# Kernel tuning notes

Measured on AMD Instinct MI355X. Metric: run time of the kernel, lower is better.

The kernel has to match this reference:

```python
import jax, jax.numpy as jnp
import numpy as np

B, N, IN_F = 8, 1024, 512
H, D = 4, 128  # num_heads, out_features; H*D == IN_F for residual
LN_EPS = 1e-5
NEG_INF = -1e9


def setup_inputs() -> dict:
    key = jax.random.key(0)
    ks = jax.random.split(key, 7)
    x = jax.random.normal(ks[0], (B, N, IN_F), dtype=jnp.float32)
    mask = jax.random.randint(ks[1], (B, N), 0, 2, dtype=jnp.int32)
    # xavier-uniform-ish init scales
    W = jax.random.uniform(ks[2], (IN_F, H * D), dtype=jnp.float32, minval=-1.0, maxval=1.0) * (1.414 * np.sqrt(6.0 / (IN_F + H * D)))
    a_src = jax.random.uniform(ks[3], (H, D), dtype=jnp.float32, minval=-1.0, maxval=1.0) * (1.414 * np.sqrt(6.0 / (H + D)))
    a_dst = jax.random.uniform(ks[4], (H, D), dtype=jnp.float32, minval=-1.0, maxval=1.0) * (1.414 * np.sqrt(6.0 / (H + D)))
    gamma = jnp.ones((H * D,), dtype=jnp.float32)
    beta = jnp.zeros((H * D,), dtype=jnp.float32)
    return {"x": x, "mask": mask, "W": W, "a_src": a_src, "a_dst": a_dst, "gamma": gamma, "beta": beta}


def _layernorm(y, gamma, beta):
    mu = jnp.mean(y, axis=-1, keepdims=True)
    var = jnp.var(y, axis=-1, keepdims=True)
    return (y - mu) * jax.lax.rsqrt(var + LN_EPS) * gamma + beta


def reference(x, mask, W, a_src, a_dst, gamma, beta):
    b, n, _ = x.shape
    h = (x @ W).reshape(b, n, H, D)                      # [B,N,H,D]
    e_i = jnp.einsum('bnhd,hd->bnh', h, a_src)           # [B,N,H]
    e_j = jnp.einsum('bnhd,hd->bnh', h, a_dst)           # [B,N,H]
    e = jax.nn.leaky_relu(e_i[:, :, None, :] + e_j[:, None, :, :], 0.2)  # [B,N,N,H]
    mm = mask[:, None, :, None] * mask[:, :, None, None]  # [B,N,N,1]
    e = jnp.where(mm == 0, NEG_INF, e)
    attn = jax.nn.softmax(e, axis=2)                     # softmax over neighbors j
    h_prime = jnp.einsum('bnjh,bjhd->bnhd', attn, h).reshape(b, n, H * D)
    return _layernorm(h_prime + x, gamma, beta)
```

## Files before the change

kernel.cpp:

```cpp
#include <hip/hip_runtime.h>
#include <math.h>

#define Bsz 8
#define Nn 1024
#define Ff 512
#define Hh 4
#define Dd 128

typedef float f32x4 __attribute__((ext_vector_type(4)));
typedef short bf16x8 __attribute__((ext_vector_type(8)));

__device__ inline uint f2b1(float a) {
    union { float f; uint u; } v; v.f = a;
    return (v.u + 0x7fffu + ((v.u >> 16) & 1u)) >> 16;
}
__device__ inline uint f2b_pk(float a, float b) { return f2b1(a) | (f2b1(b) << 16); }


__global__ __launch_bounds__(256) void conv_xw(const float* __restrict__ X,
                                               const float* __restrict__ Wm,
                                               ushort* __restrict__ Xc,
                                               ushort* __restrict__ Wc) {
    __shared__ float tile[8 * 520];
    const int bi = blockIdx.x, tid = threadIdx.x;
    if (bi < 512) {
        const int mtile = (bi & 7) * 64 + (bi >> 3);
        const int kblk = tid >> 2, m15b = (tid & 3) * 4;
        #pragma unroll
        for (int c = 0; c < 4; ++c) {
            int m15 = m15b + c;
            const float4* xp = (const float4*)(X + (size_t)(mtile * 16 + m15) * Ff + kblk * 8);
            float4 f0 = xp[0], f1 = xp[1];
            uint4 o = { f2b_pk(f0.x, f0.y), f2b_pk(f0.z, f0.w),
                        f2b_pk(f1.x, f1.y), f2b_pk(f1.z, f1.w) };
            *(uint4*)(Xc + (((size_t)(mtile * 64 + kblk) * 16 + m15) << 3)) = o;
        }
    } else {
        const int kb = bi - 512;
        const int l = tid & 63, wv = tid >> 6;
        const int col0 = l * 8;
        #pragma unroll
        for (int rsel = 0; rsel < 2; ++rsel) {
            int kr = wv + rsel * 4;
            const float4* wp = (const float4*)(Wm + (size_t)(kb * 8 + kr) * Ff + col0);
            float4 a = wp[0], c = wp[1];
            *(float4*)(&tile[kr * 520 + col0]) = a;
            *(float4*)(&tile[kr * 520 + col0 + 4]) = c;
        }
        __syncthreads();
        #pragma unroll
        for (int rsel = 0; rsel < 2; ++rsel) {
            int n = tid + rsel * 256;
            float v[8];
            #pragma unroll
            for (int u = 0; u < 8; ++u) v[u] = tile[u * 520 + n];
            uint4 o = { f2b_pk(v[0], v[1]), f2b_pk(v[2], v[3]),
                        f2b_pk(v[4], v[5]), f2b_pk(v[6], v[7]) };
            int nc = n >> 7, nt = (n >> 4) & 7, n15 = n & 15;
            *(uint4*)(Wc + ((size_t)(((nc * 64 + kb) * 8 + nt) * 16 + n15) << 3)) = o;
        }
    }
}

__global__ __launch_bounds__(256, 2) void gemm_xw(const ushort* __restrict__ Xc,
                                                  const ushort* __restrict__ Wc,
                                                  const float* __restrict__ a_src,
                                                  const float* __restrict__ a_dst,
                                                  ushort* __restrict__ hT,
                                                  float* __restrict__ ei,
                                                  float* __restrict__ ej) {
    const int idx = blockIdx.x;
    const int b = idx & 7, sub = idx >> 3;
    const int mi = sub & 15, nc = sub >> 4;
    const int tid = threadIdx.x;
    const int w = tid >> 6, lane = tid & 63, quad = lane >> 4, l16 = lane & 15;
    const int mtile = (b * 16 + mi) * 4 + w;

    f32x4 z = {0.f, 0.f, 0.f, 0.f};
    f32x4 acc[8];
    #pragma unroll
    for (int nt = 0; nt < 8; ++nt) acc[nt] = z;

    const ushort* ap = Xc + ((size_t)mtile << 13) + quad * 128 + l16 * 8;
    const ushort* bp = Wc + ((size_t)nc << 16) + quad * 1024 + l16 * 8;

    bf16x8 ab[2];
    bf16x8 bb[2][8];
    ab[0] = *(const bf16x8*)(ap);
    ab[1] = *(const bf16x8*)(ap + 512);
    #pragma unroll
    for (int nt = 0; nt < 8; ++nt) {
        bb[0][nt] = *(const bf16x8*)(bp + nt * 128);
        bb[1][nt] = *(const bf16x8*)(bp + 4096 + nt * 128);
    }

    #pragma unroll 2
    for (int s = 0; s < 16; ++s) {
        const int c = s & 1;
        #pragma unroll
        for (int nt = 0; nt < 8; ++nt)
            acc[nt] = __builtin_amdgcn_mfma_f32_16x16x32_bf16(ab[c], bb[c][nt], acc[nt], 0, 0, 0);
        if (s + 2 < 16) {
            ab[c] = *(const bf16x8*)(ap + (s + 2) * 512);
            #pragma unroll
            for (int nt = 0; nt < 8; ++nt)
                bb[c][nt] = *(const bf16x8*)(bp + (s + 2) * 4096 + nt * 128);
        }
    }

    const int nseq = (mi * 4 + w) * 16 + quad * 4;
    const int jb = nseq >> 5, js = nseq & 31;
    #pragma unroll
    for (int nt = 0; nt < 8; ++nt) {
        uint2 pv;
        pv.x = f2b_pk(acc[nt][0], acc[nt][1]);
        pv.y = f2b_pk(acc[nt][2], acc[nt][3]);
        int hd = nc * 128 + nt * 16 + l16;
        *(uint2*)(hT + ((size_t)(b * 32 + jb)) * 16384 + (size_t)hd * 32 + js) = pv;
    }

    {
        float as4[8], ad4[8];
        #pragma unroll
        for (int nt = 0; nt < 8; ++nt) {
            as4[nt] = a_src[nc * 128 + nt * 16 + l16];
            ad4[nt] = a_dst[nc * 128 + nt * 16 + l16];
        }
        #pragma unroll
        for (int rr = 0; rr < 4; ++rr) {
            float v1 = 0.f, v2 = 0.f;
            #pragma unroll
            for (int nt = 0; nt < 8; ++nt) {
                v1 += acc[nt][rr] * as4[nt];
                v2 += acc[nt][rr] * ad4[nt];
            }
            #pragma unroll
            for (int off = 1; off < 16; off <<= 1) {
                v1 += __shfl_xor(v1, off);
                v2 += __shfl_xor(v2, off);
            }
            if (l16 == 0) {
                int n = nseq + rr;
                ei[((b * 4 + nc) << 10) + n] = v1;
                ej[((b * 4 + nc) << 10) + n] = v2;
            }
        }
    }
}

__global__ __launch_bounds__(512, 2) void attn_pv(const ushort* __restrict__ hT,
                                                  const float* __restrict__ ei_g,
                                                  const float* __restrict__ ej_g,
                                                  const int* __restrict__ mask,
                                                  const float* __restrict__ X,
                                                  const float* __restrict__ gamma,
                                                  const float* __restrict__ beta,
                                                  float* __restrict__ out) {
    __shared__ float s_ep[32 * 516];
    __shared__ float s_as[4][32];

    const int idx = blockIdx.x;
    const int b = idx & 7, i0 = (idx >> 3) * 32;
    const int tid = threadIdx.x;
    const int w = tid >> 6, w4 = w & 3, jh = w >> 2;
    const int lane = tid & 63, quad = lane >> 4, l16 = lane & 15;

    const float* ejh = ej_g + ((b * 4 + w4) << 10);
    const int* mkb = mask + (b << 10);

    float maxej = -3.0e38f;
    #pragma unroll
    for (int k = 0; k < 16; ++k) maxej = fmaxf(maxej, ejh[lane + 64 * k]);
    #pragma unroll
    for (int off = 1; off < 64; off <<= 1) maxej = fmaxf(maxej, __shfl_xor(maxej, off));

    const float ei0 = ei_g[((b * 4 + w4) << 10) + i0 + l16];
    const float ei1 = ei_g[((b * 4 + w4) << 10) + i0 + 16 + l16];
    const int mi0 = mkb[i0 + l16];
    const int mi1 = mkb[i0 + 16 + l16];
    float m0, m1;
    { float t = ei0 + maxej; m0 = mi0 ? fmaxf(t, 0.2f * t) : -1e9f; }
    { float t = ei1 + maxej; m1 = mi1 ? fmaxf(t, 0.2f * t) : -1e9f; }

    f32x4 z = {0.f, 0.f, 0.f, 0.f};
    f32x4 acc[2][8], asum[2];
    #pragma unroll
    for (int it = 0; it < 2; ++it) { asum[it] = z;
        #pragma unroll
        for (int dt = 0; dt < 8; ++dt) acc[it][dt] = z; }
    bf16x8 ones;
    #pragma unroll
    for (int q = 0; q < 8; ++q) ones[q] = (short)0x3F80;

    const ushort* hTb = hT + ((size_t)(b * 32)) * 16384 + (size_t)(w4 * 128) * 32
                        + l16 * 32 + quad * 8;

    bf16x8 B[2][8];
    #pragma unroll
    for (int c = 0; c < 2; ++c) {
        const ushort* h0 = hTb + (size_t)(jh * 16 + c) * 16384;
        #pragma unroll
        for (int dt = 0; dt < 8; ++dt) B[c][dt] = *(const bf16x8*)(h0 + dt * 512);
    }

    #pragma unroll 2
    for (int r = 0; r < 16; ++r) {
        const int c = r & 1;
        const int jq = (jh * 16 + r) * 32 + quad * 8;
        float4 e0 = *(const float4*)(ejh + jq);
        float4 e1 = *(const float4*)(ejh + jq + 4);
        int4 q0 = *(const int4*)(mkb + jq);
        int4 q1 = *(const int4*)(mkb + jq + 4);
        float ev[8] = {e0.x, e0.y, e0.z, e0.w, e1.x, e1.y, e1.z, e1.w};
        int   mv[8] = {q0.x, q0.y, q0.z, q0.w, q1.x, q1.y, q1.z, q1.w};
        float wv0[8], wv1[8];
        #pragma unroll
        for (int u = 0; u < 8; ++u) {
            float t0 = ei0 + ev[u];
            float l0 = fmaxf(t0, 0.2f * t0);
            wv0[u] = __expf(((mi0 && mv[u]) ? l0 : -1e9f) - m0);
            float t1 = ei1 + ev[u];
            float l1 = fmaxf(t1, 0.2f * t1);
            wv1[u] = __expf(((mi1 && mv[u]) ? l1 : -1e9f) - m1);
        }
        union { uint4 u; bf16x8 v; } af0, af1;
        af0.u.x = f2b_pk(wv0[0], wv0[1]); af0.u.y = f2b_pk(wv0[2], wv0[3]);
        af0.u.z = f2b_pk(wv0[4], wv0[5]); af0.u.w = f2b_pk(wv0[6], wv0[7]);
        af1.u.x = f2b_pk(wv1[0], wv1[1]); af1.u.y = f2b_pk(wv1[2], wv1[3]);
        af1.u.z = f2b_pk(wv1[4], wv1[5]); af1.u.w = f2b_pk(wv1[6], wv1[7]);
        asum[0] = __builtin_amdgcn_mfma_f32_16x16x32_bf16(af0.v, ones, asum[0], 0, 0, 0);
        asum[1] = __builtin_amdgcn_mfma_f32_16x16x32_bf16(af1.v, ones, asum[1], 0, 0, 0);
        #pragma unroll
        for (int dt = 0; dt < 8; ++dt) {
            acc[0][dt] = __builtin_amdgcn_mfma_f32_16x16x32_bf16(af0.v, B[c][dt], acc[0][dt], 0, 0, 0);
            acc[1][dt] = __builtin_amdgcn_mfma_f32_16x16x32_bf16(af1.v, B[c][dt], acc[1][dt], 0, 0, 0);
        }
        if (r + 2 < 16) {
            const ushort* hn = hTb + (size_t)(jh * 16 + r + 2) * 16384;
            #pragma unroll
            for (int dt = 0; dt < 8; ++dt) B[c][dt] = *(const bf16x8*)(hn + dt * 512);
        }
    }

    if (jh == 1) {
        #pragma unroll
        for (int it = 0; it < 2; ++it)
            #pragma unroll
            for (int dt = 0; dt < 8; ++dt)
                #pragma unroll
                for (int rr = 0; rr < 4; ++rr)
                    s_ep[(it * 16 + quad * 4 + rr) * 516 + w4 * 128 + dt * 16 + l16] =
                        acc[it][dt][rr];
        if (l16 == 0) {
            #pragma unroll
            for (int it = 0; it < 2; ++it)
                #pragma unroll
                for (int rr = 0; rr < 4; ++rr)
                    s_as[w4][it * 16 + quad * 4 + rr] = asum[it][rr];
        }
    }
    __syncthreads();
    if (jh == 0) {
        float rs[2][4];
        #pragma unroll
        for (int it = 0; it < 2; ++it)
            #pragma unroll
            for (int rr = 0; rr < 4; ++rr)
                rs[it][rr] = 1.f / (asum[it][rr] + s_as[w4][it * 16 + quad * 4 + rr]);
        #pragma unroll
        for (int it = 0; it < 2; ++it)
            #pragma unroll
            for (int dt = 0; dt < 8; ++dt)
                #pragma unroll
                for (int rr = 0; rr < 4; ++rr) {
                    int off = (it * 16 + quad * 4 + rr) * 516 + w4 * 128 + dt * 16 + l16;
                    s_ep[off] = (acc[it][dt][rr] + s_ep[off]) * rs[it][rr];
                }
    }
    __syncthreads();

    #pragma unroll
    for (int q = 0; q < 4; ++q) {
        int ir = w * 4 + q;
        int ig = i0 + ir;
        float4 p0 = *(const float4*)(&s_ep[ir * 516 + lane * 8]);
        float4 p1 = *(const float4*)(&s_ep[ir * 516 + lane * 8 + 4]);
        const float* xp = X + (((size_t)((b << 10) + ig)) << 9) + lane * 8;
        float4 x0 = *(const float4*)(xp);
        float4 x1 = *(const float4*)(xp + 4);
        float v[8] = {p0.x + x0.x, p0.y + x0.y, p0.z + x0.z, p0.w + x0.w,
                      p1.x + x1.x, p1.y + x1.y, p1.z + x1.z, p1.w + x1.w};
        float s1 = 0.f, s2 = 0.f;
        #pragma unroll
        for (int u = 0; u < 8; ++u) { s1 += v[u]; s2 += v[u] * v[u]; }
        #pragma unroll
        for (int off = 1; off < 64; off <<= 1) { s1 += __shfl_xor(s1, off); s2 += __shfl_xor(s2, off); }
        float mean = s1 * (1.f / 512.f);
        float var  = s2 * (1.f / 512.f) - mean * mean;
        float rstd = rsqrtf(var + 1e-5f);
        int f0i = lane * 8;
        float4 g0 = *(const float4*)(gamma + f0i);
        float4 g1 = *(const float4*)(gamma + f0i + 4);
        float4 be0 = *(const float4*)(beta + f0i);
        float4 be1 = *(const float4*)(beta + f0i + 4);
        float* op = out + (((size_t)((b << 10) + ig)) << 9) + f0i;
        float4 o0, o1;
        o0.x = (v[0] - mean) * rstd * g0.x + be0.x;
        o0.y = (v[1] - mean) * rstd * g0.y + be0.y;
        o0.z = (v[2] - mean) * rstd * g0.z + be0.z;
        o0.w = (v[3] - mean) * rstd * g0.w + be0.w;
        o1.x = (v[4] - mean) * rstd * g1.x + be1.x;
        o1.y = (v[5] - mean) * rstd * g1.y + be1.y;
        o1.z = (v[6] - mean) * rstd * g1.z + be1.z;
        o1.w = (v[7] - mean) * rstd * g1.w + be1.w;
        *(float4*)op = o0;
        *(float4*)(op + 4) = o1;
    }
}

extern "C" void kernel_launch(void* const* d_in, const int* in_sizes, int n_in,
                              void* d_out, int out_size, void* d_ws, size_t ws_size,
                              hipStream_t stream) {
    const float* x     = (const float*)d_in[0];
    const int*   mask  = (const int*)d_in[1];
    const float* W     = (const float*)d_in[2];
    const float* a_src = (const float*)d_in[3];
    const float* a_dst = (const float*)d_in[4];
    const float* gamma = (const float*)d_in[5];
    const float* beta  = (const float*)d_in[6];
    float* out = (float*)d_out;

    ushort* hT = (ushort*)d_ws;
    ushort* Xc = hT + (size_t)8 * 512 * 1024;
    ushort* Wc = Xc + (size_t)8 * 1024 * 512;
    float* ei = (float*)(Wc + (size_t)512 * 512);
    float* ej = ei + 32768;

    conv_xw<<<dim3(576), 256, 0, stream>>>(x, W, Xc, Wc);
    gemm_xw<<<dim3(512), 256, 0, stream>>>(Xc, Wc, a_src, a_dst, hT, ei, ej);
    attn_pv<<<dim3(256), 512, 0, stream>>>(hT, ei, ej, mask, x, gamma, beta, out);
}
```

Before: 125.9 us.

## Fuse three kernels into one cooperative kernel with grid syncs

Result: slower. 204.9 us (+62.8%).

```diff
diff --git a/kernel.cpp b/kernel.cpp
--- a/kernel.cpp
+++ b/kernel.cpp
@@ -1,5 +1,8 @@
 #include <hip/hip_runtime.h>
+#include <hip/hip_cooperative_groups.h>
 #include <math.h>
+
+namespace cg = cooperative_groups;
 
 #define Bsz 8
 #define Nn 1024
@@ -17,15 +20,33 @@
 __device__ inline uint f2b_pk(float a, float b) { return f2b1(a) | (f2b1(b) << 16); }
 
 
-__global__ __launch_bounds__(256) void conv_xw(const float* __restrict__ X,
-                                               const float* __restrict__ Wm,
-                                               ushort* __restrict__ Xc,
-                                               ushort* __restrict__ Wc) {
+__global__ __launch_bounds__(512, 2) void fused_gat(const float* __restrict__ X,
+                                                    const int*   __restrict__ mask,
+                                                    const float* __restrict__ Wm,
+                                                    const float* __restrict__ a_src,
+                                                    const float* __restrict__ a_dst,
+                                                    const float* __restrict__ gamma,
+                                                    const float* __restrict__ beta,
+                                                    float* __restrict__ out,
+                                                    ushort* __restrict__ hT,
+                                                    ushort* __restrict__ Xc,
+                                                    ushort* __restrict__ Wc,
+                                                    float* __restrict__ ei_g,
+                                                    float* __restrict__ ej_g) {
     __shared__ float tile[8 * 520];
-    const int bi = blockIdx.x, tid = threadIdx.x;
-    if (bi < 512) {
-        const int mtile = (bi & 7) * 64 + (bi >> 3);
-        const int kblk = tid >> 2, m15b = (tid & 3) * 4;
+    __shared__ float s_ep[32 * 516];
+    __shared__ float s_as[4][32];
+
+    cg::grid_group grid = cg::this_grid();
+    const int idx = blockIdx.x;
+    const int tid = threadIdx.x;
+    const int b = idx & 7;
+
+    {
+        const int s = idx >> 3;
+        const int half = tid >> 8, t = tid & 255;
+        const int mtile = b * 64 + s * 2 + half;
+        const int kblk = t >> 2, m15b = (t & 3) * 4;
         #pragma unroll
         for (int c = 0; c < 4; ++c) {
             int m15 = m15b + c;
@@ -35,22 +56,15 @@
                         f2b_pk(f1.x, f1.y), f2b_pk(f1.z, f1.w) };
             *(uint4*)(Xc + (((size_t)(mtile * 64 + kblk) * 16 + m15) << 3)) = o;
         }
-    } else {
-        const int kb = bi - 512;
-        const int l = tid & 63, wv = tid >> 6;
-        const int col0 = l * 8;
-        #pragma unroll
-        for (int rsel = 0; rsel < 2; ++rsel) {
-            int kr = wv + rsel * 4;
+        if (idx < 64) {
+            const int kb = idx;
+            const int kr = tid >> 6, col0 = (tid & 63) * 8;
             const float4* wp = (const float4*)(Wm + (size_t)(kb * 8 + kr) * Ff + col0);
             float4 a = wp[0], c = wp[1];
             *(float4*)(&tile[kr * 520 + col0]) = a;
             *(float4*)(&tile[kr * 520 + col0 + 4]) = c;
-        }
-        __syncthreads();
-        #pragma unroll
-        for (int rsel = 0; rsel < 2; ++rsel) {
-            int n = tid + rsel * 256;
+            __syncthreads();
+            const int n = tid;
             float v[8];
             #pragma unroll
             for (int u = 0; u < 8; ++u) v[u] = tile[u * 520 + n];
@@ -60,261 +74,244 @@
             *(uint4*)(Wc + ((size_t)(((nc * 64 + kb) * 8 + nt) * 16 + n15) << 3)) = o;
         }
     }
-}
-
-__global__ __launch_bounds__(256, 2) void gemm_xw(const ushort* __restrict__ Xc,
-                                                  const ushort* __restrict__ Wc,
-                                                  const float* __restrict__ a_src,
-                                                  const float* __restrict__ a_dst,
-                                                  ushort* __restrict__ hT,
-                                                  float* __restrict__ ei,
-                                                  float* __restrict__ ej) {
-    const int idx = blockIdx.x;
-    const int b = idx & 7, sub = idx >> 3;
-    const int mi = sub & 15, nc = sub >> 4;
-    const int tid = threadIdx.x;
-    const int w = tid >> 6, lane = tid & 63, quad = lane >> 4, l16 = lane & 15;
-    const int mtile = (b * 16 + mi) * 4 + w;
-
-    f32x4 z = {0.f, 0.f, 0.f, 0.f};
-    f32x4 acc[8];
-    #pragma unroll
-    for (int nt = 0; nt < 8; ++nt) acc[nt] = z;
-
-    const ushort* ap = Xc + ((size_t)mtile << 13) + quad * 128 + l16 * 8;
-    const ushort* bp = Wc + ((size_t)nc << 16) + quad * 1024 + l16 * 8;
-
-    bf16x8 ab[2];
-    bf16x8 bb[2][8];
-    ab[0] = *(const bf16x8*)(ap);
-    ab[1] = *(const bf16x8*)(ap + 512);
-    #pragma unroll
-    for (int nt = 0; nt < 8; ++nt) {
-        bb[0][nt] = *(const bf16x8*)(bp + nt * 128);
-        bb[1][nt] = *(const bf16x8*)(bp + 4096 + nt * 128);
+    grid.sync();
+
+    {
+        const int w8 = tid >> 6;
+        const int lane = tid & 63, quad = lane >> 4, l16 = lane & 15;
+        const int mi = (idx >> 3) & 15, ncp = idx >> 7;
+        const int nc = ncp * 2 + (w8 >> 2), w = w8 & 3;
+        const int mtile = (b * 16 + mi) * 4 + w;
+
+        f32x4 z = {0.f, 0.f, 0.f, 0.f};
+        f32x4 acc[8];
+        #pragma unroll
+        for (int nt = 0; nt < 8; ++nt) acc[nt] = z;
+
+        const ushort* ap = Xc + ((size_t)mtile << 13) + quad * 128 + l16 * 8;
+        const ushort* bp = Wc + ((size_t)nc << 16) + quad * 1024 + l16 * 8;
+
+        bf16x8 ab[2];
+        bf16x8 bb[2][8];
+        ab[0] = *(const bf16x8*)(ap);
+        ab[1] = *(const bf16x8*)(ap + 512);
+        #pragma unroll
+        for (int nt = 0; nt < 8; ++nt) {
+            bb[0][nt] = *(const bf16x8*)(bp + nt * 128);
+            bb[1][nt] = *(const bf16x8*)(bp + 4096 + nt * 128);
+        }
+
+        #pragma unroll 2
+        for (int s = 0; s < 16; ++s) {
+            const int c = s & 1;
+            #pragma unroll
+            for (int nt = 0; nt < 8; ++nt)
+                acc[nt] = __builtin_amdgcn_mfma_f32_16x16x32_bf16(ab[c], bb[c][nt], acc[nt], 0, 0, 0);
+            if (s + 2 < 16) {
+                ab[c] = *(const bf16x8*)(ap + (s + 2) * 512);
+                #pragma unroll
+                for (int nt = 0; nt < 8; ++nt)
+                    bb[c][nt] = *(const bf16x8*)(bp + (s + 2) * 4096 + nt * 128);
+            }
+        }
+
+        const int nseq = (mi * 4 + w) * 16 + quad * 4;
+        const int jb = nseq >> 5, js = nseq & 31;
+        #pragma unroll
+        for (int nt = 0; nt < 8; ++nt) {
+            uint2 pv;
+            pv.x = f2b_pk(acc[nt][0], acc[nt][1]);
+            pv.y = f2b_pk(acc[nt][2], acc[nt][3]);
+            int hd = nc * 128 + nt * 16 + l16;
+            *(uint2*)(hT + ((size_t)(b * 32 + jb)) * 16384 + (size_t)hd * 32 + js) = pv;
+        }
+
+        {
+            float as4[8], ad4[8];
+            #pragma unroll
+            for (int nt = 0; nt < 8; ++nt) {
+                as4[nt] = a_src[nc * 128 + nt * 16 + l16];
+                ad4[nt] = a_dst[nc * 128 + nt * 16 + l16];
+            }
+            #pragma unroll
+            for (int rr = 0; rr < 4; ++rr) {
+                float v1 = 0.f, v2 = 0.f;
+                #pragma unroll
+                for (int nt = 0; nt < 8; ++nt) {
+                    v1 += acc[nt][rr] * as4[nt];
+                    v2 += acc[nt][rr] * ad4[nt];
+                }
+                #pragma unroll
+                for (int off = 1; off < 16; off <<= 1) {
+                    v1 += __shfl_xor(v1, off);
+                    v2 += __shfl_xor(v2, off);
+                }
+                if (l16 == 0) {
+                    int n = nseq + rr;
+                    ei_g[((b * 4 + nc) << 10) + n] = v1;
+                    ej_g[((b * 4 + nc) << 10) + n] = v2;
+                }
+            }
+        }
     }
-
-    #pragma unroll 2
-    for (int s = 0; s < 16; ++s) {
-        const int c = s & 1;
-        #pragma unroll
-        for (int nt = 0; nt < 8; ++nt)
-            acc[nt] = __builtin_amdgcn_mfma_f32_16x16x32_bf16(ab[c], bb[c][nt], acc[nt], 0, 0, 0);
-        if (s + 2 < 16) {
-            ab[c] = *(const bf16x8*)(ap + (s + 2) * 512);
-            #pragma unroll
-            for (int nt = 0; nt < 8; ++nt)
-                bb[c][nt] = *(const bf16x8*)(bp + (s + 2) * 4096 + nt * 128);
-        }
-    }
-
-    const int nseq = (mi * 4 + w) * 16 + quad * 4;
-    const int jb = nseq >> 5, js = nseq & 31;
-    #pragma unroll
-    for (int nt = 0; nt < 8; ++nt) {
-        uint2 pv;
-        pv.x = f2b_pk(acc[nt][0], acc[nt][1]);
-        pv.y = f2b_pk(acc[nt][2], acc[nt][3]);
-        int hd = nc * 128 + nt * 16 + l16;
-        *(uint2*)(hT + ((size_t)(b * 32 + jb)) * 16384 + (size_t)hd * 32 + js) = pv;
-    }
+    grid.sync();
 
     {
-        float as4[8], ad4[8];
-        #pragma unroll
-        for (int nt = 0; nt < 8; ++nt) {
-            as4[nt] = a_src[nc * 128 + nt * 16 + l16];
-            ad4[nt] = a_dst[nc * 128 + nt * 16 + l16];
-        }
-        #pragma unroll
-        for (int rr = 0; rr < 4; ++rr) {
-            float v1 = 0.f, v2 = 0.f;
-            #pragma unroll
-            for (int nt = 0; nt < 8; ++nt) {
-                v1 += acc[nt][rr] * as4[nt];
-                v2 += acc[nt][rr] * ad4[nt];
-            }
-            #pragma unroll
-            for (int off = 1; off < 16; off <<= 1) {
-                v1 += __shfl_xor(v1, off);
-                v2 += __shfl_xor(v2, off);
-            }
+        const int i0 = (idx >> 3) * 32;
+        const int w = tid >> 6, w4 = w & 3, jh = w >> 2;
+        const int lane = tid & 63, quad = lane >> 4, l16 = lane & 15;
+
+        const float* ejh = ej_g + ((b * 4 + w4) << 10);
+        const int* mkb = mask + (b << 10);
+
+        float maxej = -3.0e38f;
+        #pragma unroll
+        for (int k = 0; k < 16; ++k) maxej = fmaxf(maxej, ejh[lane + 64 * k]);
+        #pragma unroll
+        for (int off = 1; off < 64; off <<= 1) maxej = fmaxf(maxej, __shfl_xor(maxej, off));
+
+        const float ei0 = ei_g[((b * 4 + w4) << 10) + i0 + l16];
+        const float ei1 = ei_g[((b * 4 + w4) << 10) + i0 + 16 + l16];
+        const int mi0 = mkb[i0 + l16];
+        const int mi1 = mkb[i0 + 16 + l16];
+        float m0, m1;
+        { float t = ei0 + maxej; m0 = mi0 ? fmaxf(t, 0.2f * t) : -1e9f; }
+        { float t = ei1 + maxej; m1 = mi1 ? fmaxf(t, 0.2f * t) : -1e9f; }
+
+        f32x4 z = {0.f, 0.f, 0.f, 0.f};
+        f32x4 acc[2][8], asum[2];
+        #pragma unroll
+        for (int it = 0; it < 2; ++it) { asum[it] = z;
+            #pragma unroll
+            for (int dt = 0; dt < 8; ++dt) acc[it][dt] = z; }
+        bf16x8 ones;
+        #pragma unroll
+        for (int q = 0; q < 8; ++q) ones[q] = (short)0x3F80;
+
+        const ushort* hTb = hT + ((size_t)(b * 32)) * 16384 + (size_t)(w4 * 128) * 32
+                            + l16 * 32 + quad * 8;
+
+        bf16x8 B[2][8];
+        #pragma unroll
+        for (int c = 0; c < 2; ++c) {
+            const ushort* h0 = hTb + (size_t)(jh * 16 + c) * 16384;
+            #pragma unroll
+            for (int dt = 0; dt < 8; ++dt) B[c][dt] = *(const bf16x8*)(h0 + dt * 512);
+        }
+
+        #pragma unroll 2
+        for (int r = 0; r < 16; ++r) {
+            const int c = r & 1;
+            const int jq = (jh * 16 + r) * 32 + quad * 8;
+            float4 e0 = *(const float4*)(ejh + jq);
+            float4 e1 = *(const float4*)(ejh + jq + 4);
+            int4 q0 = *(const int4*)(mkb + jq);
+            int4 q1 = *(const int4*)(mkb + jq + 4);
+            float ev[8] = {e0.x, e0.y, e0.z, e0.w, e1.x, e1.y, e1.z, e1.w};
+            int   mv[8] = {q0.x, q0.y, q0.z, q0.w, q1.x, q1.y, q1.z, q1.w};
+            float wv0[8], wv1[8];
+            #pragma unroll
+            for (int u = 0; u < 8; ++u) {
+                float t0 = ei0 + ev[u];
+                float l0 = fmaxf(t0, 0.2f * t0);
+                wv0[u] = __expf(((mi0 && mv[u]) ? l0 : -1e9f) - m0);
+                float t1 = ei1 + ev[u];
+                float l1 = fmaxf(t1, 0.2f * t1);
+                wv1[u] = __expf(((mi1 && mv[u]) ? l1 : -1e9f) - m1);
+            }
+            union { uint4 u; bf16x8 v; } af0, af1;
+            af0.u.x = f2b_pk(wv0[0], wv0[1]); af0.u.y = f2b_pk(wv0[2], wv0[3]);
+            af0.u.z = f2b_pk(wv0[4], wv0[5]); af0.u.w = f2b_pk(wv0[6], wv0[7]);
+            af1.u.x = f2b_pk(wv1[0], wv1[1]); af1.u.y = f2b_pk(wv1[2], wv1[3]);
+            af1.u.z = f2b_pk(wv1[4], wv1[5]); af1.u.w = f2b_pk(wv1[6], wv1[7]);
+            asum[0] = __builtin_amdgcn_mfma_f32_16x16x32_bf16(af0.v, ones, asum[0], 0, 0, 0);
+            asum[1] = __builtin_amdgcn_mfma_f32_16x16x32_bf16(af1.v, ones, asum[1], 0, 0, 0);
+            #pragma unroll
+            for (int dt = 0; dt < 8; ++dt) {
+                acc[0][dt] = __builtin_amdgcn_mfma_f32_16x16x32_bf16(af0.v, B[c][dt], acc[0][dt], 0, 0, 0);
+                acc[1][dt] = __builtin_amdgcn_mfma_f32_16x16x32_bf16(af1.v, B[c][dt], acc[1][dt], 0, 0, 0);
+            }
+            if (r + 2 < 16) {
+                const ushort* hn = hTb + (size_t)(jh * 16 + r + 2) * 16384;
+                #pragma unroll
+                for (int dt = 0; dt < 8; ++dt) B[c][dt] = *(const bf16x8*)(hn + dt * 512);
+            }
+        }
+
+        if (jh == 1) {
+            #pragma unroll
+            for (int it = 0; it < 2; ++it)
+                #pragma unroll
+                for (int dt = 0; dt < 8; ++dt)
+                    #pragma unroll
+                    for (int rr = 0; rr < 4; ++rr)
+                        s_ep[(it * 16 + quad * 4 + rr) * 516 + w4 * 128 + dt * 16 + l16] =
+                            acc[it][dt][rr];
             if (l16 == 0) {
-                int n = nseq + rr;
-                ei[((b * 4 + nc) << 10) + n] = v1;
-                ej[((b * 4 + nc) << 10) + n] = v2;
-            }
-        }
-    }
-}
-
-__global__ __launch_bounds__(512, 2) void attn_pv(const ushort* __restrict__ hT,
-                                                  const float* __restrict__ ei_g,
-                                                  const float* __restrict__ ej_g,
-                                                  const int* __restrict__ mask,
-                                                  const float* __restrict__ X,
-                                                  const float* __restrict__ gamma,
-                                                  const float* __restrict__ beta,
-                                                  float* __restrict__ out) {
-    __shared__ float s_ep[32 * 516];
-    __shared__ float s_as[4][32];
-
-    const int idx = blockIdx.x;
-    const int b = idx & 7, i0 = (idx >> 3) * 32;
-    const int tid = threadIdx.x;
-    const int w = tid >> 6, w4 = w & 3, jh = w >> 2;
-    const int lane = tid & 63, quad = lane >> 4, l16 = lane & 15;
-
-    const float* ejh = ej_g + ((b * 4 + w4) << 10);
-    const int* mkb = mask + (b << 10);
-
-    float maxej = -3.0e38f;
-    #pragma unroll
-    for (int k = 0; k < 16; ++k) maxej = fmaxf(maxej, ejh[lane + 64 * k]);
-    #pragma unroll
-    for (int off = 1; off < 64; off <<= 1) maxej = fmaxf(maxej, __shfl_xor(maxej, off));
-
-    const float ei0 = ei_g[((b * 4 + w4) << 10) + i0 + l16];
-    const float ei1 = ei_g[((b * 4 + w4) << 10) + i0 + 16 + l16];
-    const int mi0 = mkb[i0 + l16];
-    const int mi1 = mkb[i0 + 16 + l16];
-    float m0, m1;
-    { float t = ei0 + maxej; m0 = mi0 ? fmaxf(t, 0.2f * t) : -1e9f; }
-    { float t = ei1 + maxej; m1 = mi1 ? fmaxf(t, 0.2f * t) : -1e9f; }
-
-    f32x4 z = {0.f, 0.f, 0.f, 0.f};
-    f32x4 acc[2][8], asum[2];
-    #pragma unroll
-    for (int it = 0; it < 2; ++it) { asum[it] = z;
-        #pragma unroll
-        for (int dt = 0; dt < 8; ++dt) acc[it][dt] = z; }
-    bf16x8 ones;
-    #pragma unroll
-    for (int q = 0; q < 8; ++q) ones[q] = (short)0x3F80;
-
-    const ushort* hTb = hT + ((size_t)(b * 32)) * 16384 + (size_t)(w4 * 128) * 32
-                        + l16 * 32 + quad * 8;
-
-    bf16x8 B[2][8];
-    #pragma unroll
-    for (int c = 0; c < 2; ++c) {
-        const ushort* h0 = hTb + (size_t)(jh * 16 + c) * 16384;
-        #pragma unroll
-        for (int dt = 0; dt < 8; ++dt) B[c][dt] = *(const bf16x8*)(h0 + dt * 512);
-    }
-
-    #pragma unroll 2
-    for (int r = 0; r < 16; ++r) {
-        const int c = r & 1;
-        const int jq = (jh * 16 + r) * 32 + quad * 8;
-        float4 e0 = *(const float4*)(ejh + jq);
-        float4 e1 = *(const float4*)(ejh + jq + 4);
-        int4 q0 = *(const int4*)(mkb + jq);
-        int4 q1 = *(const int4*)(mkb + jq + 4);
-        float ev[8] = {e0.x, e0.y, e0.z, e0.w, e1.x, e1.y, e1.z, e1.w};
-        int   mv[8] = {q0.x, q0.y, q0.z, q0.w, q1.x, q1.y, q1.z, q1.w};
-        float wv0[8], wv1[8];
-        #pragma unroll
-        for (int u = 0; u < 8; ++u) {
-            float t0 = ei0 + ev[u];
-            float l0 = fmaxf(t0, 0.2f * t0);
-            wv0[u] = __expf(((mi0 && mv[u]) ? l0 : -1e9f) - m0);
-            float t1 = ei1 + ev[u];
-            float l1 = fmaxf(t1, 0.2f * t1);
-            wv1[u] = __expf(((mi1 && mv[u]) ? l1 : -1e9f) - m1);
-        }
-        union { uint4 u; bf16x8 v; } af0, af1;
-        af0.u.x = f2b_pk(wv0[0], wv0[1]); af0.u.y = f2b_pk(wv0[2], wv0[3]);
-        af0.u.z = f2b_pk(wv0[4], wv0[5]); af0.u.w = f2b_pk(wv0[6], wv0[7]);
-        af1.u.x = f2b_pk(wv1[0], wv1[1]); af1.u.y = f2b_pk(wv1[2], wv1[3]);
-        af1.u.z = f2b_pk(wv1[4], wv1[5]); af1.u.w = f2b_pk(wv1[6], wv1[7]);
-        asum[0] = __builtin_amdgcn_mfma_f32_16x16x32_bf16(af0.v, ones, asum[0], 0, 0, 0);
-        asum[1] = __builtin_amdgcn_mfma_f32_16x16x32_bf16(af1.v, ones, asum[1], 0, 0, 0);
-        #pragma unroll
-        for (int dt = 0; dt < 8; ++dt) {
-            acc[0][dt] = __builtin_amdgcn_mfma_f32_16x16x32_bf16(af0.v, B[c][dt], acc[0][dt], 0, 0, 0);
-            acc[1][dt] = __builtin_amdgcn_mfma_f32_16x16x32_bf16(af1.v, B[c][dt], acc[1][dt], 0, 0, 0);
-        }
-        if (r + 2 < 16) {
-            const ushort* hn = hTb + (size_t)(jh * 16 + r + 2) * 16384;
-            #pragma unroll
-            for (int dt = 0; dt < 8; ++dt) B[c][dt] = *(const bf16x8*)(hn + dt * 512);
-        }
-    }
-
-    if (jh == 1) {
-        #pragma unroll
-        for (int it = 0; it < 2; ++it)
-            #pragma unroll
-            for (int dt = 0; dt < 8; ++dt)
+                #pragma unroll
+                for (int it = 0; it < 2; ++it)
+                    #pragma unroll
+                    for (int rr = 0; rr < 4; ++rr)
+                        s_as[w4][it * 16 + quad * 4 + rr] = asum[it][rr];
+            }
+        }
+        __syncthreads();
+        if (jh == 0) {
+            float rs[2][4];
+            #pragma unroll
+            for (int it = 0; it < 2; ++it)
                 #pragma unroll
                 for (int rr = 0; rr < 4; ++rr)
-                    s_ep[(it * 16 + quad * 4 + rr) * 516 + w4 * 128 + dt * 16 + l16] =
-                        acc[it][dt][rr];
-        if (l16 == 0) {
+                    rs[it][rr] = 1.f / (asum[it][rr] + s_as[w4][it * 16 + quad * 4 + rr]);
             #pragma unroll
             for (int it = 0; it < 2; ++it)
                 #pragma unroll
-                for (int rr = 0; rr < 4; ++rr)
-                    s_as[w4][it * 16 + quad * 4 + rr] = asum[it][rr];
-        }
-    }
-    __syncthreads();
-    if (jh == 0) {
-        float rs[2][4];
-        #pragma unroll
-        for (int it = 0; it < 2; ++it)
-            #pragma unroll
-            for (int rr = 0; rr < 4; ++rr)
-                rs[it][rr] = 1.f / (asum[it][rr] + s_as[w4][it * 16 + quad * 4 + rr]);
-        #pragma unroll
-        for (int it = 0; it < 2; ++it)
-            #pragma unroll
-            for (int dt = 0; dt < 8; ++dt)
-                #pragma unroll
-                for (int rr = 0; rr < 4; ++rr) {
-                    int off = (it * 16 + quad * 4 + rr) * 516 + w4 * 128 + dt * 16 + l16;
-                    s_ep[off] = (acc[it][dt][rr] + s_ep[off]) * rs[it][rr];
-                }
-    }
-    __syncthreads();
-
-    #pragma unroll
-    for (int q = 0; q < 4; ++q) {
-        int ir = w * 4 + q;
-        int ig = i0 + ir;
-        float4 p0 = *(const float4*)(&s_ep[ir * 516 + lane * 8]);
-        float4 p1 = *(const float4*)(&s_ep[ir * 516 + lane * 8 + 4]);
-        const float* xp = X + (((size_t)((b << 10) + ig)) << 9) + lane * 8;
-        float4 x0 = *(const float4*)(xp);
-        float4 x1 = *(const float4*)(xp + 4);
-        float v[8] = {p0.x + x0.x, p0.y + x0.y, p0.z + x0.z, p0.w + x0.w,
-                      p1.x + x1.x, p1.y + x1.y, p1.z + x1.z, p1.w + x1.w};
-        float s1 = 0.f, s2 = 0.f;
-        #pragma unroll
-        for (int u = 0; u < 8; ++u) { s1 += v[u]; s2 += v[u] * v[u]; }
-        #pragma unroll
-        for (int off = 1; off < 64; off <<= 1) { s1 += __shfl_xor(s1, off); s2 += __shfl_xor(s2, off); }
-        float mean = s1 * (1.f / 512.f);
-        float var  = s2 * (1.f / 512.f) - mean * mean;
-        float rstd = rsqrtf(var + 1e-5f);
-        int f0i = lane * 8;
-        float4 g0 = *(const float4*)(gamma + f0i);
-        float4 g1 = *(const float4*)(gamma + f0i + 4);
-        float4 be0 = *(const float4*)(beta + f0i);
-        float4 be1 = *(const float4*)(beta + f0i + 4);
-        float* op = out + (((size_t)((b << 10) + ig)) << 9) + f0i;
-        float4 o0, o1;
-        o0.x = (v[0] - mean) * rstd * g0.x + be0.x;
-        o0.y = (v[1] - mean) * rstd * g0.y + be0.y;
-        o0.z = (v[2] - mean) * rstd * g0.z + be0.z;
-        o0.w = (v[3] - mean) * rstd * g0.w + be0.w;
-        o1.x = (v[4] - mean) * rstd * g1.x + be1.x;
-        o1.y = (v[5] - mean) * rstd * g1.y + be1.y;
-        o1.z = (v[6] - mean) * rstd * g1.z + be1.z;
-        o1.w = (v[7] - mean) * rstd * g1.w + be1.w;
-        *(float4*)op = o0;
-        *(float4*)(op + 4) = o1;
+                for (int dt = 0; dt < 8; ++dt)
+                    #pragma unroll
+                    for (int rr = 0; rr < 4; ++rr) {
+                        int off = (it * 16 + quad * 4 + rr) * 516 + w4 * 128 + dt * 16 + l16;
+                        s_ep[off] = (acc[it][dt][rr] + s_ep[off]) * rs[it][rr];
+                    }
+        }
+        __syncthreads();
+
+        #pragma unroll
+        for (int q = 0; q < 4; ++q) {
+            int ir = w * 4 + q;
+            int ig = i0 + ir;
+            float4 p0 = *(const float4*)(&s_ep[ir * 516 + lane * 8]);
+            float4 p1 = *(const float4*)(&s_ep[ir * 516 + lane * 8 + 4]);
+            const float* xp = X + (((size_t)((b << 10) + ig)) << 9) + lane * 8;
+            float4 x0 = *(const float4*)(xp);
+            float4 x1 = *(const float4*)(xp + 4);
+            float v[8] = {p0.x + x0.x, p0.y + x0.y, p0.z + x0.z, p0.w + x0.w,
+                          p1.x + x1.x, p1.y + x1.y, p1.z + x1.z, p1.w + x1.w};
+            float s1 = 0.f, s2 = 0.f;
+            #pragma unroll
+            for (int u = 0; u < 8; ++u) { s1 += v[u]; s2 += v[u] * v[u]; }
+            #pragma unroll
+            for (int off = 1; off < 64; off <<= 1) { s1 += __shfl_xor(s1, off); s2 += __shfl_xor(s2, off); }
+            float mean = s1 * (1.f / 512.f);
+            float var  = s2 * (1.f / 512.f) - mean * mean;
+            float rstd = rsqrtf(var + 1e-5f);
+            int f0i = lane * 8;
+            float4 g0 = *(const float4*)(gamma + f0i);
+            float4 g1 = *(const float4*)(gamma + f0i + 4);
+            float4 be0 = *(const float4*)(beta + f0i);
+            float4 be1 = *(const float4*)(beta + f0i + 4);
+            float* op = out + (((size_t)((b << 10) + ig)) << 9) + f0i;
+            float4 o0, o1;
+            o0.x = (v[0] - mean) * rstd * g0.x + be0.x;
+            o0.y = (v[1] - mean) * rstd * g0.y + be0.y;
+            o0.z = (v[2] - mean) * rstd * g0.z + be0.z;
+            o0.w = (v[3] - mean) * rstd * g0.w + be0.w;
+            o1.x = (v[4] - mean) * rstd * g1.x + be1.x;
+            o1.y = (v[5] - mean) * rstd * g1.y + be1.y;
+            o1.z = (v[6] - mean) * rstd * g1.z + be1.z;
+            o1.w = (v[7] - mean) * rstd * g1.w + be1.w;
+            *(float4*)op = o0;
+            *(float4*)(op + 4) = o1;
+        }
     }
 }
 
@@ -336,7 +333,9 @@
     float* ei = (float*)(Wc + (size_t)512 * 512);
     float* ej = ei + 32768;
 
-    conv_xw<<<dim3(576), 256, 0, stream>>>(x, W, Xc, Wc);
-    gemm_xw<<<dim3(512), 256, 0, stream>>>(Xc, Wc, a_src, a_dst, hT, ei, ej);
-    attn_pv<<<dim3(256), 512, 0, stream>>>(hT, ei, ej, mask, x, gamma, beta, out);
+    void* args[] = { (void*)&x, (void*)&mask, (void*)&W, (void*)&a_src, (void*)&a_dst,
+                     (void*)&gamma, (void*)&beta, (void*)&out, (void*)&hT, (void*)&Xc,
+                     (void*)&Wc, (void*)&ei, (void*)&ej };
+    hipLaunchCooperativeKernel((const void*)fused_gat, dim3(256), dim3(512),
+                               args, 0, stream);
 }
```
